# Kernel optimization log

Measured on AMD Instinct MI355X. Metric: run time of the kernel, lower is better.

The kernel has to match this reference:

```python
import jax, jax.numpy as jnp
import numpy as np

B, S, D_IN, D_EMB = 8, 2048, 512, 512

def setup_inputs() -> dict:
    key = jax.random.key(0)
    ks = jax.random.split(key, 7)
    s = 1.0 / np.sqrt(D_IN)
    return {
        "x": jax.random.normal(ks[0], (B, S, D_IN), dtype=jnp.float32),
        "Wq": jax.random.uniform(ks[1], (D_IN, D_EMB), jnp.float32, -s, s),
        "bq": jax.random.uniform(ks[2], (D_EMB,), jnp.float32, -s, s),
        "Wk": jax.random.uniform(ks[3], (D_IN, D_EMB), jnp.float32, -s, s),
        "bk": jax.random.uniform(ks[4], (D_EMB,), jnp.float32, -s, s),
        "Wv": jax.random.uniform(ks[5], (D_IN, D_EMB), jnp.float32, -s, s),
        "bv": jax.random.uniform(ks[6], (D_EMB,), jnp.float32, -s, s),
    }

def reference(x, Wq, bq, Wk, bk, Wv, bv):
    # single-head attention: softmax(QK^T / sqrt(d)) V
    q = x @ Wq + bq            # [B,S,E]
    k = x @ Wk + bk
    v = x @ Wv + bv
    scores = jnp.einsum('bse,bte->bst', q, k) / jnp.sqrt(jnp.float32(D_EMB))
    attn = jax.nn.softmax(scores, axis=-1)  # [B,S,S]
    return jnp.einsum('bst,bte->bse', attn, v)
```

## Files before the change

kernel.cpp:

```cpp
#include <hip/hip_runtime.h>
#include <stdint.h>


using f32x4 = __attribute__((ext_vector_type(4))) float;
using s16x8 = __attribute__((ext_vector_type(8))) short;
using u16x4 = __attribute__((ext_vector_type(4))) unsigned short;

#define S_LEN 2048
#define EMB   512

#define ASYNC16(g, l)                                                     \
  __builtin_amdgcn_global_load_lds(                                       \
      (const __attribute__((address_space(1))) void*)(g),                 \
      (__attribute__((address_space(3))) void*)(l), 16, 0, 0)

__device__ __forceinline__ unsigned short f2bf(float f) {
  union { float f; unsigned u; } v; v.f = f;
  unsigned r = v.u + 0x7fffu + ((v.u >> 16) & 1u);
  return (unsigned short)(r >> 16);
}

__global__ __launch_bounds__(256) void xconv_kernel(
    const float* __restrict__ x, short* __restrict__ xb) {
  int i = (blockIdx.x * 256 + threadIdx.x) * 8;
  f32x4 a = *(const f32x4*)(x + i);
  f32x4 b = *(const f32x4*)(x + i + 4);
  s16x8 h;
  h[0] = (short)f2bf(a[0]); h[1] = (short)f2bf(a[1]);
  h[2] = (short)f2bf(a[2]); h[3] = (short)f2bf(a[3]);
  h[4] = (short)f2bf(b[0]); h[5] = (short)f2bf(b[1]);
  h[6] = (short)f2bf(b[2]); h[7] = (short)f2bf(b[3]);
  *(s16x8*)(xb + i) = h;
}

__global__ __launch_bounds__(256) void wconv_kernel(
    const float* __restrict__ Wq, const float* __restrict__ Wk,
    const float* __restrict__ Wv, short* __restrict__ Wt) {
  __shared__ float T[64][65];
  int bid = blockIdx.x;
  int mat = bid >> 6;
  int t   = bid & 63;
  int k0  = (t & 7) << 6, n0 = (t >> 3) << 6;
  const float* W = (mat == 0) ? Wq : (mat == 1) ? Wk : Wv;
  int tid = threadIdx.x;
  int rr = tid >> 4, cc = tid & 15;
#pragma unroll
  for (int p = 0; p < 4; ++p) {
    int row = p * 16 + rr;
    f32x4 v = *(const f32x4*)(W + (size_t)(k0 + row) * 512 + n0 + cc * 4);
#pragma unroll
    for (int j = 0; j < 4; ++j) T[row][cc * 4 + j] = v[j];
  }
  __syncthreads();
  short* D = Wt + (size_t)mat * 262144;
#pragma unroll
  for (int p = 0; p < 4; ++p) {
    int nrow = p * 16 + rr;
    u16x4 h;
#pragma unroll
    for (int j = 0; j < 4; ++j) h[j] = f2bf(T[cc * 4 + j][nrow]);
    *(u16x4*)(D + (size_t)(n0 + nrow) * 512 + k0 + cc * 4) = h;
  }
}

__global__ __launch_bounds__(256) void qkv_gemm(
    const short* __restrict__ xb, const short* __restrict__ Wt,
    const float* __restrict__ bq, const float* __restrict__ bk,
    const float* __restrict__ bv,
    short* __restrict__ Qg, short* __restrict__ Kg, short* __restrict__ VTg) {
  __shared__ __align__(16) short As[2][128 * 64];
  __shared__ __align__(16) short Bs[2][128 * 64];
  int gid = blockIdx.x;
  int mat = gid >> 9;
  int rem = gid & 511;
  int mt  = rem & 127, nt = rem >> 7;
  int m0  = mt << 7,   n0 = nt << 7;
  const short* W    = Wt + (size_t)mat * 262144;
  const float* bias = (mat == 0) ? bq : (mat == 1) ? bk : bv;

  int tid = threadIdx.x, lane = tid & 63, wv = tid >> 6;
  int l16 = lane & 15, quad = lane >> 4;
  int wr = (wv & 1) << 6, wc = (wv >> 1) << 6;
  int drow = lane >> 3;
  int dchk = (lane & 7) ^ drow;

  const short* asrc[4];
  const short* bsrc[4];
#pragma unroll
  for (int i = 0; i < 4; ++i) {
    int row = (wv * 4 + i) * 8 + drow;
    asrc[i] = xb + (size_t)(m0 + row) * 512 + dchk * 8;
    bsrc[i] = W  + (size_t)(n0 + row) * 512 + dchk * 8;
  }

  const f32x4 Z4 = {0.f, 0.f, 0.f, 0.f};
  f32x4 acc[4][4];
#pragma unroll
  for (int a = 0; a < 4; ++a)
#pragma unroll
    for (int c = 0; c < 4; ++c) acc[a][c] = Z4;

#pragma unroll
  for (int i = 0; i < 4; ++i) {
    int g = wv * 4 + i;
    ASYNC16(asrc[i], &As[0][g * 512]);
    ASYNC16(bsrc[i], &Bs[0][g * 512]);
  }
  __syncthreads();

  for (int it = 0; it < 8; ++it) {
    int buf = it & 1;
    if (it < 7) {
      int k1 = (it + 1) << 6;
#pragma unroll
      for (int i = 0; i < 4; ++i) {
        int g = wv * 4 + i;
        ASYNC16(asrc[i] + k1, &As[buf ^ 1][g * 512]);
        ASYNC16(bsrc[i] + k1, &Bs[buf ^ 1][g * 512]);
      }
    }
#pragma unroll
    for (int kk = 0; kk < 2; ++kk) {
      s16x8 af[4], bfr[4];
#pragma unroll
      for (int rb = 0; rb < 4; ++rb) {
        int row = wr + rb * 16 + l16;
        int c   = kk * 4 + quad;
        af[rb] = *(const s16x8*)(&As[buf][row * 64 + ((c ^ (row & 7)) * 8)]);
      }
#pragma unroll
      for (int cb = 0; cb < 4; ++cb) {
        int row = wc + cb * 16 + l16;
        int c   = kk * 4 + quad;
        bfr[cb] = *(const s16x8*)(&Bs[buf][row * 64 + ((c ^ (row & 7)) * 8)]);
      }
#pragma unroll
      for (int rb = 0; rb < 4; ++rb)
#pragma unroll
        for (int cb = 0; cb < 4; ++cb)
          acc[rb][cb] = __builtin_amdgcn_mfma_f32_16x16x32_bf16(af[rb], bfr[cb], acc[rb][cb], 0, 0, 0);
    }
    __syncthreads();
  }

  float bsv[4];
#pragma unroll
  for (int cb = 0; cb < 4; ++cb) bsv[cb] = bias[n0 + wc + cb * 16 + l16];

  if (mat < 2) {
    short* D = (mat == 0) ? Qg : Kg;
#pragma unroll
    for (int rb = 0; rb < 4; ++rb)
#pragma unroll
      for (int cb = 0; cb < 4; ++cb)
#pragma unroll
        for (int r = 0; r < 4; ++r) {
          int m = m0 + wr + rb * 16 + quad * 4 + r;
          D[(size_t)m * 512 + n0 + wc + cb * 16 + l16] =
              (short)f2bf(acc[rb][cb][r] + bsv[cb]);
        }
  } else {
#pragma unroll
    for (int rb = 0; rb < 4; ++rb)
#pragma unroll
      for (int cb = 0; cb < 4; ++cb) {
        u16x4 h;
#pragma unroll
        for (int r = 0; r < 4; ++r) h[r] = f2bf(acc[rb][cb][r] + bsv[cb]);
        int m  = m0 + wr + rb * 16 + quad * 4;
        int bb = m >> 11, sl = m & 2047;
        int e  = n0 + wc + cb * 16 + l16;
        size_t idx = ((((size_t)bb * 32 + (e >> 4)) * 64 + (sl >> 5)) * 16 +
                      (e & 15)) * 32 + (sl & 31);
        *(u16x4*)(VTg + idx) = h;
      }
  }
}

__global__ __launch_bounds__(512, 2) void attn_kernel(
    const short* __restrict__ Qg, const short* __restrict__ Kg,
    const short* __restrict__ VTg, float* __restrict__ out) {
  __shared__ __align__(16) short Kt[3][32 * 512];
  __shared__ __align__(16) short Pl[2][64 * 40];
  __shared__ float l_l[64];
  const float SCL2 = 0.06375871855f;

  int b = blockIdx.x & 7, qt = blockIdx.x >> 3;
  int s0 = qt << 6;
  int tid = threadIdx.x, lane = tid & 63, wv = tid >> 6;
  int l16 = lane & 15, quad = lane >> 4;
  int a = wv & 3, h = wv >> 2;
  int e0 = wv << 6;

  const short* Kb = Kg  + (size_t)b * S_LEN * 512;
  const short* Vb = VTg + (size_t)b * 1048576;

  const short* kdma[4];
#pragma unroll
  for (int i = 0; i < 4; ++i) {
    int r = wv * 4 + i;
    kdma[i] = Kb + (size_t)r * 512 + ((lane ^ (r & 7)) * 8);
  }
  const short* vbase = Vb + (size_t)wv * 131072 + l16 * 32 + quad * 8;

#pragma unroll
  for (int i = 0; i < 4; ++i)
    ASYNC16(kdma[i], &Kt[0][(wv * 4 + i) * 512]);
#pragma unroll
  for (int i = 0; i < 4; ++i)
    ASYNC16(kdma[i] + 16384, &Kt[1][(wv * 4 + i) * 512]);

  const short* qrow = Qg + ((size_t)b * S_LEN + s0 + a * 16 + l16) * 512 + quad * 8;
  s16x8 qf[16];
#pragma unroll
  for (int kk = 0; kk < 16; ++kk) qf[kk] = *(const s16x8*)(qrow + kk * 32);

  const f32x4 Z4 = {0.f, 0.f, 0.f, 0.f};
  f32x4 acc[4][4];
#pragma unroll
  for (int rb = 0; rb < 4; ++rb)
#pragma unroll
    for (int cb = 0; cb < 4; ++cb) acc[rb][cb] = Z4;
  f32x4 lsum = Z4;

  __syncthreads();

  int rbuf = 0, wbuf = 2;
  for (int kt = 0; kt < 64; ++kt) {
    s16x8 vf[4];
#pragma unroll
    for (int cb = 0; cb < 4; ++cb)
      vf[cb] = *(const s16x8*)(vbase + (size_t)cb * 32768 + (size_t)kt * 512);
    __builtin_amdgcn_sched_barrier(0);

    {
      size_t adv = (size_t)((kt + 2) & 63) * 16384;
#pragma unroll
      for (int i = 0; i < 4; ++i)
        ASYNC16(kdma[i] + adv, &Kt[wbuf][(wv * 4 + i) * 512]);
    }
    __builtin_amdgcn_sched_barrier(0);

    f32x4 s_a = Z4, s_b = Z4;
    int krow = h * 16 + l16;
    const short* kb = &Kt[rbuf][krow * 512];
    int ksw = krow & 7;
    __builtin_amdgcn_s_setprio(1);
#pragma unroll
    for (int kk = 0; kk < 8; ++kk) {
      s16x8 kf0 = *(const s16x8*)(kb + (((2 * kk) * 4 + quad) ^ ksw) * 8);
      s_a = __builtin_amdgcn_mfma_f32_16x16x32_bf16(qf[2 * kk], kf0, s_a, 0, 0, 0);
      s16x8 kf1 = *(const s16x8*)(kb + (((2 * kk + 1) * 4 + quad) ^ ksw) * 8);
      s_b = __builtin_amdgcn_mfma_f32_16x16x32_bf16(qf[2 * kk + 1], kf1, s_b, 0, 0, 0);
    }
    __builtin_amdgcn_s_setprio(0);
    f32x4 sv = s_a + s_b;

    short* Pc = Pl[kt & 1];
#pragma unroll
    for (int r = 0; r < 4; ++r) {
      float p = exp2f(sv[r] * SCL2);
      lsum[r] += p;
      Pc[(a * 16 + quad * 4 + r) * 40 + h * 16 + l16] = (short)f2bf(p);
    }

    asm volatile("s_waitcnt vmcnt(8) lgkmcnt(0)\n\ts_barrier" ::: "memory");

    s16x8 pf[4];
#pragma unroll
    for (int g = 0; g < 4; ++g)
      pf[g] = *(const s16x8*)(Pc + (g * 16 + l16) * 40 + quad * 8);
    __builtin_amdgcn_s_setprio(1);
#pragma unroll
    for (int cb = 0; cb < 4; ++cb)
#pragma unroll
      for (int g = 0; g < 4; ++g)
        acc[g][cb] = __builtin_amdgcn_mfma_f32_16x16x32_bf16(pf[g], vf[cb], acc[g][cb], 0, 0, 0);
    __builtin_amdgcn_s_setprio(0);

    rbuf = (rbuf == 2) ? 0 : rbuf + 1;
    wbuf = (wbuf == 2) ? 0 : wbuf + 1;
  }

#pragma unroll
  for (int r = 0; r < 4; ++r) {
    float v = lsum[r];
    v += __shfl_xor(v, 1);
    v += __shfl_xor(v, 2);
    v += __shfl_xor(v, 4);
    v += __shfl_xor(v, 8);
    lsum[r] = v;
  }
  if (h == 0 && l16 == 0) {
#pragma unroll
    for (int r = 0; r < 4; ++r) l_l[a * 16 + quad * 4 + r] = lsum[r];
  }
  __syncthreads();
  if (h == 1 && l16 == 0) {
#pragma unroll
    for (int r = 0; r < 4; ++r) l_l[a * 16 + quad * 4 + r] += lsum[r];
  }
  __syncthreads();

#pragma unroll
  for (int rb = 0; rb < 4; ++rb) {
    f32x4 lv = *(const f32x4*)(l_l + rb * 16 + quad * 4);
    f32x4 li;
#pragma unroll
    for (int r = 0; r < 4; ++r) li[r] = 1.0f / lv[r];
#pragma unroll
    for (int cb = 0; cb < 4; ++cb)
#pragma unroll
      for (int r = 0; r < 4; ++r)
        out[((size_t)b * S_LEN + s0 + rb * 16 + quad * 4 + r) * 512 + e0 + cb * 16 + l16] =
            acc[rb][cb][r] * li[r];
  }
}

extern "C" void kernel_launch(void* const* d_in, const int* in_sizes, int n_in,
                              void* d_out, int out_size, void* d_ws, size_t ws_size,
                              hipStream_t stream) {
  const float* x  = (const float*)d_in[0];
  const float* Wq = (const float*)d_in[1];
  const float* bq = (const float*)d_in[2];
  const float* Wk = (const float*)d_in[3];
  const float* bk = (const float*)d_in[4];
  const float* Wv = (const float*)d_in[5];
  const float* bv = (const float*)d_in[6];

  short* Wt  = (short*)d_ws;
  short* xb  = (short*)((char*)d_ws + 1572864);
  short* Qg  = xb + (size_t)8388608;
  short* Kg  = Qg + (size_t)8388608;
  short* VTg = Kg + (size_t)8388608;

  xconv_kernel<<<4096, 256, 0, stream>>>(x, xb);
  wconv_kernel<<<192, 256, 0, stream>>>(Wq, Wk, Wv, Wt);
  qkv_gemm<<<1536, 256, 0, stream>>>(xb, Wt, bq, bk, bv, Qg, Kg, VTg);
  attn_kernel<<<256, 512, 0, stream>>>(Qg, Kg, VTg, (float*)d_out);
}
```

Baseline: 240.8 us.

## Merge conversion kernels, vectorize Q/K epilogue, retile attention to 32-row query blocks

Combines the x and weight conversion kernels into one launch to save a launch. In the QKV GEMM, swaps the MFMA operands for Q and K so each lane holds four consecutive columns, which allows vectorized 4-wide bf16 stores and a vector bias load. The attention kernel is retiled to 32-query blocks with 4 waves of 256 threads, each wave covering 128 output columns, with double-buffered instead of triple-buffered K tiles and twice the blocks. This raises block count and cuts LDS per block, but each block reloads K and V for fewer queries, so global traffic per output doubles, and the shallower K prefetch may expose latency.

```diff
diff --git a/kernel.cpp b/kernel.cpp
--- a/kernel.cpp
+++ b/kernel.cpp
@@ -20,46 +20,46 @@
   return (unsigned short)(r >> 16);
 }
 
-__global__ __launch_bounds__(256) void xconv_kernel(
-    const float* __restrict__ x, short* __restrict__ xb) {
-  int i = (blockIdx.x * 256 + threadIdx.x) * 8;
-  f32x4 a = *(const f32x4*)(x + i);
-  f32x4 b = *(const f32x4*)(x + i + 4);
-  s16x8 h;
-  h[0] = (short)f2bf(a[0]); h[1] = (short)f2bf(a[1]);
-  h[2] = (short)f2bf(a[2]); h[3] = (short)f2bf(a[3]);
-  h[4] = (short)f2bf(b[0]); h[5] = (short)f2bf(b[1]);
-  h[6] = (short)f2bf(b[2]); h[7] = (short)f2bf(b[3]);
-  *(s16x8*)(xb + i) = h;
-}
-
-__global__ __launch_bounds__(256) void wconv_kernel(
+__global__ __launch_bounds__(256) void conv_kernel(
+    const float* __restrict__ x, short* __restrict__ xb,
     const float* __restrict__ Wq, const float* __restrict__ Wk,
     const float* __restrict__ Wv, short* __restrict__ Wt) {
   __shared__ float T[64][65];
-  int bid = blockIdx.x;
-  int mat = bid >> 6;
-  int t   = bid & 63;
-  int k0  = (t & 7) << 6, n0 = (t >> 3) << 6;
-  const float* W = (mat == 0) ? Wq : (mat == 1) ? Wk : Wv;
-  int tid = threadIdx.x;
-  int rr = tid >> 4, cc = tid & 15;
-#pragma unroll
-  for (int p = 0; p < 4; ++p) {
-    int row = p * 16 + rr;
-    f32x4 v = *(const f32x4*)(W + (size_t)(k0 + row) * 512 + n0 + cc * 4);
-#pragma unroll
-    for (int j = 0; j < 4; ++j) T[row][cc * 4 + j] = v[j];
-  }
-  __syncthreads();
-  short* D = Wt + (size_t)mat * 262144;
-#pragma unroll
-  for (int p = 0; p < 4; ++p) {
-    int nrow = p * 16 + rr;
-    u16x4 h;
-#pragma unroll
-    for (int j = 0; j < 4; ++j) h[j] = f2bf(T[cc * 4 + j][nrow]);
-    *(u16x4*)(D + (size_t)(n0 + nrow) * 512 + k0 + cc * 4) = h;
+  if (blockIdx.x < 4096) {
+    int i = (blockIdx.x * 256 + threadIdx.x) * 8;
+    f32x4 a = *(const f32x4*)(x + i);
+    f32x4 b = *(const f32x4*)(x + i + 4);
+    s16x8 h;
+    h[0] = (short)f2bf(a[0]); h[1] = (short)f2bf(a[1]);
+    h[2] = (short)f2bf(a[2]); h[3] = (short)f2bf(a[3]);
+    h[4] = (short)f2bf(b[0]); h[5] = (short)f2bf(b[1]);
+    h[6] = (short)f2bf(b[2]); h[7] = (short)f2bf(b[3]);
+    *(s16x8*)(xb + i) = h;
+  } else {
+    int bid = blockIdx.x - 4096;
+    int mat = bid >> 6;
+    int t   = bid & 63;
+    int k0  = (t & 7) << 6, n0 = (t >> 3) << 6;
+    const float* W = (mat == 0) ? Wq : (mat == 1) ? Wk : Wv;
+    int tid = threadIdx.x;
+    int rr = tid >> 4, cc = tid & 15;
+#pragma unroll
+    for (int p = 0; p < 4; ++p) {
+      int row = p * 16 + rr;
+      f32x4 v = *(const f32x4*)(W + (size_t)(k0 + row) * 512 + n0 + cc * 4);
+#pragma unroll
+      for (int j = 0; j < 4; ++j) T[row][cc * 4 + j] = v[j];
+    }
+    __syncthreads();
+    short* D = Wt + (size_t)mat * 262144;
+#pragma unroll
+    for (int p = 0; p < 4; ++p) {
+      int nrow = p * 16 + rr;
+      u16x4 h;
+#pragma unroll
+      for (int j = 0; j < 4; ++j) h[j] = f2bf(T[cc * 4 + j][nrow]);
+      *(u16x4*)(D + (size_t)(n0 + nrow) * 512 + k0 + cc * 4) = h;
+    }
   }
 }
 
@@ -134,32 +134,42 @@
         int c   = kk * 4 + quad;
         bfr[cb] = *(const s16x8*)(&Bs[buf][row * 64 + ((c ^ (row & 7)) * 8)]);
       }
-#pragma unroll
-      for (int rb = 0; rb < 4; ++rb)
-#pragma unroll
-        for (int cb = 0; cb < 4; ++cb)
-          acc[rb][cb] = __builtin_amdgcn_mfma_f32_16x16x32_bf16(af[rb], bfr[cb], acc[rb][cb], 0, 0, 0);
+      if (mat < 2) {
+#pragma unroll
+        for (int rb = 0; rb < 4; ++rb)
+#pragma unroll
+          for (int cb = 0; cb < 4; ++cb)
+            acc[rb][cb] = __builtin_amdgcn_mfma_f32_16x16x32_bf16(bfr[cb], af[rb], acc[rb][cb], 0, 0, 0);
+      } else {
+#pragma unroll
+        for (int rb = 0; rb < 4; ++rb)
+#pragma unroll
+          for (int cb = 0; cb < 4; ++cb)
+            acc[rb][cb] = __builtin_amdgcn_mfma_f32_16x16x32_bf16(af[rb], bfr[cb], acc[rb][cb], 0, 0, 0);
+      }
     }
     __syncthreads();
   }
-
-  float bsv[4];
-#pragma unroll
-  for (int cb = 0; cb < 4; ++cb) bsv[cb] = bias[n0 + wc + cb * 16 + l16];
 
   if (mat < 2) {
     short* D = (mat == 0) ? Qg : Kg;
 #pragma unroll
-    for (int rb = 0; rb < 4; ++rb)
-#pragma unroll
-      for (int cb = 0; cb < 4; ++cb)
-#pragma unroll
-        for (int r = 0; r < 4; ++r) {
-          int m = m0 + wr + rb * 16 + quad * 4 + r;
-          D[(size_t)m * 512 + n0 + wc + cb * 16 + l16] =
-              (short)f2bf(acc[rb][cb][r] + bsv[cb]);
-        }
+    for (int cb = 0; cb < 4; ++cb) {
+      f32x4 bv4 = *(const f32x4*)(bias + n0 + wc + cb * 16 + quad * 4);
+#pragma unroll
+      for (int rb = 0; rb < 4; ++rb) {
+        u16x4 h;
+#pragma unroll
+        for (int r = 0; r < 4; ++r) h[r] = f2bf(acc[rb][cb][r] + bv4[r]);
+        int m = m0 + wr + rb * 16 + l16;
+        int e = n0 + wc + cb * 16 + quad * 4;
+        *(u16x4*)(D + (size_t)m * 512 + e) = h;
+      }
+    }
   } else {
+    float bsv[4];
+#pragma unroll
+    for (int cb = 0; cb < 4; ++cb) bsv[cb] = bias[n0 + wc + cb * 16 + l16];
 #pragma unroll
     for (int rb = 0; rb < 4; ++rb)
 #pragma unroll
@@ -177,38 +187,35 @@
   }
 }
 
-__global__ __launch_bounds__(512, 2) void attn_kernel(
+__global__ __launch_bounds__(256, 2) void attn_kernel(
     const short* __restrict__ Qg, const short* __restrict__ Kg,
     const short* __restrict__ VTg, float* __restrict__ out) {
-  __shared__ __align__(16) short Kt[3][32 * 512];
-  __shared__ __align__(16) short Pl[2][64 * 40];
-  __shared__ float l_l[64];
+  __shared__ __align__(16) short Kt[2][32 * 512];
+  __shared__ __align__(16) short Pl[2][32 * 40];
+  __shared__ float l_l[32];
   const float SCL2 = 0.06375871855f;
 
   int b = blockIdx.x & 7, qt = blockIdx.x >> 3;
-  int s0 = qt << 6;
+  int s0 = qt << 5;
   int tid = threadIdx.x, lane = tid & 63, wv = tid >> 6;
   int l16 = lane & 15, quad = lane >> 4;
-  int a = wv & 3, h = wv >> 2;
-  int e0 = wv << 6;
+  int a = wv & 1, h = wv >> 1;
+  int e0 = wv << 7;
 
   const short* Kb = Kg  + (size_t)b * S_LEN * 512;
   const short* Vb = VTg + (size_t)b * 1048576;
 
-  const short* kdma[4];
-#pragma unroll
-  for (int i = 0; i < 4; ++i) {
-    int r = wv * 4 + i;
-    kdma[i] = Kb + (size_t)r * 512 + ((lane ^ (r & 7)) * 8);
-  }
-  const short* vbase = Vb + (size_t)wv * 131072 + l16 * 32 + quad * 8;
-
-#pragma unroll
-  for (int i = 0; i < 4; ++i)
-    ASYNC16(kdma[i], &Kt[0][(wv * 4 + i) * 512]);
-#pragma unroll
-  for (int i = 0; i < 4; ++i)
-    ASYNC16(kdma[i] + 16384, &Kt[1][(wv * 4 + i) * 512]);
+  const short* kdma[8];
+#pragma unroll
+  for (int i = 0; i < 8; ++i) {
+    int r = wv * 8 + i;
+    kdma[i] = Kb + (size_t)r * 512 + ((lane ^ i) * 8);
+  }
+  const short* vbase = Vb + (size_t)wv * 262144 + l16 * 32 + quad * 8;
+
+#pragma unroll
+  for (int i = 0; i < 8; ++i)
+    ASYNC16(kdma[i], &Kt[0][(wv * 8 + i) * 512]);
 
   const short* qrow = Qg + ((size_t)b * S_LEN + s0 + a * 16 + l16) * 512 + quad * 8;
   s16x8 qf[16];
@@ -216,34 +223,35 @@
   for (int kk = 0; kk < 16; ++kk) qf[kk] = *(const s16x8*)(qrow + kk * 32);
 
   const f32x4 Z4 = {0.f, 0.f, 0.f, 0.f};
-  f32x4 acc[4][4];
-#pragma unroll
-  for (int rb = 0; rb < 4; ++rb)
-#pragma unroll
-    for (int cb = 0; cb < 4; ++cb) acc[rb][cb] = Z4;
+  f32x4 acc[2][8];
+#pragma unroll
+  for (int g = 0; g < 2; ++g)
+#pragma unroll
+    for (int cb = 0; cb < 8; ++cb) acc[g][cb] = Z4;
   f32x4 lsum = Z4;
 
   __syncthreads();
 
-  int rbuf = 0, wbuf = 2;
   for (int kt = 0; kt < 64; ++kt) {
-    s16x8 vf[4];
-#pragma unroll
-    for (int cb = 0; cb < 4; ++cb)
+    int buf = kt & 1;
+
+    {
+      size_t adv = (size_t)((kt + 1) & 63) * 16384;
+#pragma unroll
+      for (int i = 0; i < 8; ++i)
+        ASYNC16(kdma[i] + adv, &Kt[buf ^ 1][(wv * 8 + i) * 512]);
+    }
+    __builtin_amdgcn_sched_barrier(0);
+
+    s16x8 vf[8];
+#pragma unroll
+    for (int cb = 0; cb < 8; ++cb)
       vf[cb] = *(const s16x8*)(vbase + (size_t)cb * 32768 + (size_t)kt * 512);
     __builtin_amdgcn_sched_barrier(0);
 
-    {
-      size_t adv = (size_t)((kt + 2) & 63) * 16384;
-#pragma unroll
-      for (int i = 0; i < 4; ++i)
-        ASYNC16(kdma[i] + adv, &Kt[wbuf][(wv * 4 + i) * 512]);
-    }
-    __builtin_amdgcn_sched_barrier(0);
-
     f32x4 s_a = Z4, s_b = Z4;
     int krow = h * 16 + l16;
-    const short* kb = &Kt[rbuf][krow * 512];
+    const short* kb = &Kt[buf][krow * 512];
     int ksw = krow & 7;
     __builtin_amdgcn_s_setprio(1);
 #pragma unroll
@@ -256,7 +264,7 @@
     __builtin_amdgcn_s_setprio(0);
     f32x4 sv = s_a + s_b;
 
-    short* Pc = Pl[kt & 1];
+    short* Pc = Pl[buf];
 #pragma unroll
     for (int r = 0; r < 4; ++r) {
       float p = exp2f(sv[r] * SCL2);
@@ -266,20 +274,17 @@
 
     asm volatile("s_waitcnt vmcnt(8) lgkmcnt(0)\n\ts_barrier" ::: "memory");
 
-    s16x8 pf[4];
-#pragma unroll
-    for (int g = 0; g < 4; ++g)
+    s16x8 pf[2];
+#pragma unroll
+    for (int g = 0; g < 2; ++g)
       pf[g] = *(const s16x8*)(Pc + (g * 16 + l16) * 40 + quad * 8);
     __builtin_amdgcn_s_setprio(1);
 #pragma unroll
-    for (int cb = 0; cb < 4; ++cb)
-#pragma unroll
-      for (int g = 0; g < 4; ++g)
+    for (int cb = 0; cb < 8; ++cb)
+#pragma unroll
+      for (int g = 0; g < 2; ++g)
         acc[g][cb] = __builtin_amdgcn_mfma_f32_16x16x32_bf16(pf[g], vf[cb], acc[g][cb], 0, 0, 0);
     __builtin_amdgcn_s_setprio(0);
-
-    rbuf = (rbuf == 2) ? 0 : rbuf + 1;
-    wbuf = (wbuf == 2) ? 0 : wbuf + 1;
   }
 
 #pragma unroll
@@ -303,17 +308,17 @@
   __syncthreads();
 
 #pragma unroll
-  for (int rb = 0; rb < 4; ++rb) {
-    f32x4 lv = *(const f32x4*)(l_l + rb * 16 + quad * 4);
+  for (int g = 0; g < 2; ++g) {
+    f32x4 lv = *(const f32x4*)(l_l + g * 16 + quad * 4);
     f32x4 li;
 #pragma unroll
     for (int r = 0; r < 4; ++r) li[r] = 1.0f / lv[r];
 #pragma unroll
-    for (int cb = 0; cb < 4; ++cb)
+    for (int cb = 0; cb < 8; ++cb)
 #pragma unroll
       for (int r = 0; r < 4; ++r)
-        out[((size_t)b * S_LEN + s0 + rb * 16 + quad * 4 + r) * 512 + e0 + cb * 16 + l16] =
-            acc[rb][cb][r] * li[r];
+        out[((size_t)b * S_LEN + s0 + g * 16 + quad * 4 + r) * 512 + e0 + cb * 16 + l16] =
+            acc[g][cb][r] * li[r];
   }
 }
 
@@ -334,8 +339,7 @@
   short* Kg  = Qg + (size_t)8388608;
   short* VTg = Kg + (size_t)8388608;
 
-  xconv_kernel<<<4096, 256, 0, stream>>>(x, xb);
-  wconv_kernel<<<192, 256, 0, stream>>>(Wq, Wk, Wv, Wt);
+  conv_kernel<<<4288, 256, 0, stream>>>(x, xb, Wq, Wk, Wv, Wt);
   qkv_gemm<<<1536, 256, 0, stream>>>(xb, Wt, bq, bk, bv, Qg, Kg, VTg);
-  attn_kernel<<<256, 512, 0, stream>>>(Qg, Kg, VTg, (float*)d_out);
-}
+  attn_kernel<<<512, 256, 0, stream>>>(Qg, Kg, VTg, (float*)d_out);
+}
```

Result: slower. 265.0 us (+10.0%).
